# Kernel tuning notes

Hardware: AMD Instinct MI355X
Metric: run time of the kernel (lower is better)

The kernel has to match this reference:

```python
import jax, jax.numpy as jnp
import numpy as np
from jax import lax

N = 8192

def _conv(x, w, b):
    # x: NCHW, w: OIHW, valid conv stride 1
    y = lax.conv_general_dilated(x, w, (1, 1), 'VALID',
                                 dimension_numbers=('NCHW', 'OIHW', 'NCHW'))
    return y + b[None, :, None, None]

def _maxpool2(x):
    return lax.reduce_window(x, -jnp.inf, lax.max, (1, 1, 2, 2), (1, 1, 2, 2), 'VALID')

def setup_inputs() -> dict:
    key = jax.random.key(0)
    ks = jax.random.split(key, 13)
    def rn(k, shape, scale):
        return jax.random.normal(k, shape, dtype=jnp.float32) * scale
    inp = {}
    inp['x'] = jax.random.normal(ks[0], (N, 3, 32, 32), dtype=jnp.float32)
    inp['W1'] = rn(ks[1], (6, 3, 5, 5), 0.1)
    inp['b1'] = rn(ks[2], (6,), 0.1)
    inp['W2'] = rn(ks[3], (16, 6, 5, 5), 0.08)
    inp['b2'] = rn(ks[4], (16,), 0.1)
    inp['Wf1'] = rn(ks[5], (120, 400), 0.05)
    inp['bf1'] = rn(ks[6], (120,), 0.05)
    inp['Wf2'] = rn(ks[7], (84, 120), 0.09)
    inp['bf2'] = rn(ks[8], (84,), 0.09)
    inp['Wg'] = rn(ks[9], (10, 84), 0.1)    # GATConv fc weight (no bias)
    inp['attn_l'] = rn(ks[10], (10,), 0.3)  # a_l (src)
    inp['attn_r'] = rn(ks[11], (10,), 0.3)  # a_r (dst)
    inp['bg'] = rn(ks[12], (10,), 0.1)      # GATConv output bias
    return inp

def reference(x, W1, b1, W2, b2, Wf1, bf1, Wf2, bf2, Wg, attn_l, attn_r, bg):
    # CNN feature extractor (LeNet style)
    h = _maxpool2(jax.nn.relu(_conv(x, W1, b1)))   # [N,6,14,14]
    h = _maxpool2(jax.nn.relu(_conv(h, W2, b2)))   # [N,16,5,5]
    h = h.reshape(-1, 16 * 5 * 5)                  # [N,400]
    h = jax.nn.relu(h @ Wf1.T + bf1)               # [N,120]
    h = jax.nn.relu(h @ Wf2.T + bf2)               # [N,84]
    # Single-head GAT over fully-connected graph (incl. self-loops):
    # equivalent dense formulation of DGL GATConv(84,10,1)
    z = h @ Wg.T                                    # [N,10]
    el = z @ attn_l                                 # src scores [N]
    er = z @ attn_r                                 # dst scores [N]
    # e[i,j]: edge src=j -> dst=i
    e = jax.nn.leaky_relu(er[:, None] + el[None, :], negative_slope=0.2)  # [N,N]
    alpha = jax.nn.softmax(e, axis=1)               # softmax over incoming edges
    out = alpha @ z + bg                            # [N,10]
    return out
```

## Files before the change

### kernel.cpp

```cpp
#include <hip/hip_runtime.h>
#include <hip/hip_bf16.h>

typedef _Float16 half8 __attribute__((ext_vector_type(8)));
typedef __attribute__((aligned(8))) half8 half8_a8;
typedef float floatx4 __attribute__((ext_vector_type(4)));

#define LOG2E 1.44269504088896340736f

__device__ __forceinline__ float pool4_dpp(float v) {
  int s1 = __builtin_amdgcn_update_dpp(0, __float_as_int(v), 0xB1, 0xF, 0xF, true);
  float v1 = fmaxf(v, __int_as_float(s1));
  int s2 = __builtin_amdgcn_update_dpp(0, __float_as_int(v1), 0x4E, 0xF, 0xF, true);
  return fmaxf(v1, __int_as_float(s2));
}

__global__ __launch_bounds__(256) void k_prep(const float* __restrict__ Wf1,
    const float* __restrict__ Wf2, const float* __restrict__ Wg,
    const float* __restrict__ W1, const float* __restrict__ W2,
    _Float16* __restrict__ w1f, _Float16* __restrict__ w2f,
    _Float16* __restrict__ wgf, _Float16* __restrict__ B1,
    _Float16* __restrict__ B2M) {
  const int i = blockIdx.x * 256 + threadIdx.x;
  if (i < 53248) {
    const int n = i / 416, k = i - n * 416;
    w1f[i] = (_Float16)((n < 120 && k < 400) ? Wf1[n * 400 + k] : 0.f);
  } else if (i < 65536) {
    const int j = i - 53248;
    const int n = j >> 7, k = j & 127;
    w2f[j] = (_Float16)((n < 84 && k < 120) ? Wf2[n * 120 + k] : 0.f);
  } else if (i < 67072) {
    const int g = i - 65536;
    const int n = g / 96, k = g - n * 96;
    wgf[g] = (_Float16)((n < 10 && k < 84) ? Wg[n * 84 + k] : 0.f);
  } else if (i < 73216) {
    const int g = i - 67072;
    const int n = g / 192, k = g - n * 192;
    const int co = n >> 2, cy = (n >> 1) & 1, cx = n & 1;
    const int pidx = k >> 3, j = k & 7;
    const int r = pidx >> 2, ci = pidx & 3;
    float v = 0.f;
    if (co < 6 && ci < 3) {
      const int ky = r - cy, kx = j - cx;
      if (ky >= 0 && ky < 5 && kx >= 0 && kx < 5)
        v = W1[((co * 3 + ci) * 5 + ky) * 5 + kx];
    }
    B1[g] = (_Float16)v;
  } else if (i < 77312) {
    const int g = i - 73216;
    const int n = g >> 8, k = g & 255;
    float v = 0.f;
    if (k < 240) {
      const int ci = k / 40, rem = k - ci * 40, r = rem >> 3, j = rem & 7;
      if (j < 5) v = W2[((n * 6 + ci) * 5 + r) * 5 + j];
    }
    B2M[g] = (_Float16)v;
  }
}

__global__ __launch_bounds__(256) void k_convs(const float* __restrict__ x,
    const _Float16* __restrict__ B1, const float* __restrict__ b1,
    const _Float16* __restrict__ B2M, const float* __restrict__ b2,
    _Float16* __restrict__ h2) {
  __shared__ __align__(16) char sm[35808];
  _Float16* h1L = (_Float16*)(sm + 31104);
  const int t = threadIdx.x;
  const int n0 = blockIdx.x * 2;
  const int w4 = t >> 6, lane = t & 63;
  const int l16 = lane & 15, q = lane >> 4;

  const float4* x4 = (const float4*)(x + (size_t)n0 * 3072);
  for (int i = t; i < 1536; i += 256) {
    const float4 v = x4[i];
    const int img = (i >= 768);
    const int ii = i - img * 768;
    const int ci = ii >> 8, rem2 = ii & 255;
    const int y = rem2 >> 3, c = rem2 & 7;
    union { _Float16 h[2]; unsigned u; } p01, p23;
    p01.h[0] = (_Float16)v.x; p01.h[1] = (_Float16)v.y;
    p23.h[0] = (_Float16)v.z; p23.h[1] = (_Float16)v.w;
    char* row = sm + img * 15552 + ci * 5184 + y * 80;
    *(uint2*)(row + 8 * c) = make_uint2(p01.u, p23.u);
    *(unsigned*)(row + 2596 + 8 * c) = p01.u;
    *(unsigned*)(row + 2600 + 8 * c) = p23.u;
  }
  if (t < 192) {
    const int img = t / 96, tt = t - img * 96;
    const int ci = tt >> 5, y = tt & 31;
    *(unsigned*)(sm + img * 15552 + ci * 5184 + 2596 + y * 80 + 64) = 0u;
  }
  if (t < 32) {
    const int im = t >> 4;
    h2[(size_t)(n0 + im) * 416 + 400 + (t & 15)] = (_Float16)0.f;
  }
  __syncthreads();

  {
    const int img = w4 >> 1, wl = w4 & 1;
    const int px = l16;
    const int colOff = (px & 1) ? (2596 + 4 * px) : (4 * px);
    const char* base = sm + img * 15552 + ((q == 3) ? 0 : q * 5184) + colOff;
    half8 bfr[2][6];
#pragma unroll
    for (int nt = 0; nt < 2; nt++)
#pragma unroll
      for (int kc = 0; kc < 6; kc++)
        bfr[nt][kc] =
            *(const half8*)(B1 + (size_t)(nt * 16 + l16) * 192 + kc * 32 + q * 8);
    const int co_n = l16 >> 2;
    const int co1 = 4 + co_n;
    const float bias0 = b1[co_n];
    const float bias1 = (co1 < 6) ? b1[co1] : 0.f;
    const int py0 = wl * 7;
    const int py1 = py0 + 7;
    half8 a[6];
#pragma unroll
    for (int r = 0; r < 6; r++)
      a[r] = *(const half8_a8*)(base + (2 * py0 + r) * 80);
    _Float16* dstb = h1L + img * 1176;
    const bool store_lane = (l16 & 3) == 0;
    for (int py = py0; py < py1; ++py) {
      floatx4 acc0, acc1;
#pragma unroll
      for (int r = 0; r < 4; r++) { acc0[r] = 0.f; acc1[r] = 0.f; }
#pragma unroll
      for (int kc = 0; kc < 6; kc++) {
        acc0 = __builtin_amdgcn_mfma_f32_16x16x32_f16(a[kc], bfr[0][kc], acc0, 0, 0, 0);
        acc1 = __builtin_amdgcn_mfma_f32_16x16x32_f16(a[kc], bfr[1][kc], acc1, 0, 0, 0);
      }
      if (py < py1 - 1) {
        a[0] = a[2]; a[1] = a[3]; a[2] = a[4]; a[3] = a[5];
        a[4] = *(const half8_a8*)(base + (2 * py + 6) * 80);
        a[5] = *(const half8_a8*)(base + (2 * py + 7) * 80);
      }
      float p0[4], p1[4];
#pragma unroll
      for (int r = 0; r < 4; r++) {
        p0[r] = fmaxf(pool4_dpp(acc0[r]) + bias0, 0.f);
        p1[r] = fmaxf(pool4_dpp(acc1[r]) + bias1, 0.f);
      }
      if (store_lane) {
        union { _Float16 h[2]; unsigned u; } s01, s23;
        s01.h[0] = (_Float16)p0[0]; s01.h[1] = (_Float16)p0[1];
        s23.h[0] = (_Float16)p0[2]; s23.h[1] = (_Float16)p0[3];
        _Float16* dst = dstb + co_n * 196 + py * 14 + q * 4;
        *(unsigned*)dst = s01.u;
        if (q < 3) *(unsigned*)(dst + 2) = s23.u;
        if (co1 < 6) {
          union { _Float16 h[2]; unsigned u; } t01, t23;
          t01.h[0] = (_Float16)p1[0]; t01.h[1] = (_Float16)p1[1];
          t23.h[0] = (_Float16)p1[2]; t23.h[1] = (_Float16)p1[3];
          _Float16* dst1 = dstb + co1 * 196 + py * 14 + q * 4;
          *(unsigned*)dst1 = t01.u;
          if (q < 3) *(unsigned*)(dst1 + 2) = t23.u;
        }
      }
    }
  }
  __syncthreads();

  if (t < 168) {
    const int img = t / 84, rem = t - img * 84;
    const int ci = rem / 14, y = rem - ci * 14;
    const unsigned* src = (const unsigned*)(h1L + img * 1176 + ci * 196 + y * 14);
    unsigned u[10];
#pragma unroll
    for (int k = 0; k < 7; k++) u[k] = src[k];
    u[7] = 0u; u[8] = 0u; u[9] = 0u;
    char* base = sm + img * 11136 + ci * 1856 + y * 32;
#pragma unroll
    for (int ww = 0; ww < 8; ww++) {
      *(unsigned*)(base + 4 * ww) = u[ww];
      *(unsigned*)(base + 464 + 4 * ww) = (u[ww] >> 16) | (u[ww + 1] << 16);
      *(unsigned*)(base + 928 + 4 * ww) = u[ww + 1];
      *(unsigned*)(base + 1392 + 4 * ww) = (u[ww + 1] >> 16) | (u[ww + 2] << 16);
    }
  }
  __syncthreads();

  {
    int C2[8];
#pragma unroll
    for (int kc = 0; kc < 8; kc++) {
      const int pidx = kc * 4 + q;
      C2[kc] = (pidx < 30) ? (pidx / 5) * 1856 + (pidx % 5) * 32 : 0;
    }
    half8 bfr[8];
#pragma unroll
    for (int kc = 0; kc < 8; kc++)
      bfr[kc] = *(const half8*)(B2M + (size_t)l16 * 256 + kc * 32 + q * 8);
    const float bias = b2[l16];
    for (int mt = w4; mt < 13; mt += 4) {
      const int m = min(mt * 16 + l16, 199);
      const int pos = m >> 2, cy = (m >> 1) & 1, cx = m & 1;
      const int img = pos / 25, p = pos - img * 25;
      const int py = p / 5, px = p - py * 5;
      const int h = 2 * px + cx, s = h & 3;
      const char* base =
          sm + img * 11136 + s * 464 + (2 * py + cy) * 32 + (h - s) * 2;
      half8 a[8];
#pragma unroll
      for (int kc = 0; kc < 8; kc++) a[kc] = *(const half8_a8*)(base + C2[kc]);
      floatx4 acc;
#pragma unroll
      for (int r = 0; r < 4; r++) acc[r] = 0.f;
#pragma unroll
      for (int kc = 0; kc < 8; kc++)
        acc = __builtin_amdgcn_mfma_f32_16x16x32_f16(a[kc], bfr[kc], acc, 0, 0, 0);
      const float v = fmaxf(fmaxf(acc[0], acc[1]), fmaxf(acc[2], acc[3]));
      const int posL = mt * 4 + q;
      if (posL < 50) {
        const int im = posL / 25, pp = posL - im * 25;
        h2[(size_t)(n0 + im) * 416 + l16 * 25 + pp] =
            (_Float16)fmaxf(v + bias, 0.f);
      }
    }
  }
}

__global__ __launch_bounds__(256) void k_mlp(
    const _Float16* __restrict__ h2, const _Float16* __restrict__ w1,
    const float* __restrict__ bf1, const _Float16* __restrict__ w2,
    const float* __restrict__ bf2, const _Float16* __restrict__ wg,
    const float* __restrict__ al, const float* __restrict__ ar,
    _Float16* __restrict__ zT, float* __restrict__ el, float* __restrict__ er) {
  __shared__ __align__(16) _Float16 h3s[32 * 136];
  __shared__ __align__(16) _Float16 h4s[32 * 104];
  __shared__ float zs[32 * 17];
  const int t = threadIdx.x;
  const int w = t >> 6, lane = t & 63;
  const int l16 = lane & 15, q = lane >> 4;
  const int row0 = blockIdx.x * 32;
  for (int i = t; i < 2176; i += 256) ((float*)h3s)[i] = 0.f;
  for (int i = t; i < 1664; i += 256) ((float*)h4s)[i] = 0.f;
  const int rt = w & 1, cg = w >> 1;
  const int am = row0 + rt * 16 + l16;
  floatx4 acc[4];
#pragma unroll
  for (int ct = 0; ct < 4; ct++)
#pragma unroll
    for (int r = 0; r < 4; r++) acc[ct][r] = 0.f;
  const half8* Ag = (const half8*)(h2 + (size_t)am * 416 + q * 8);
  for (int kc = 0; kc < 13; kc++) {
    half8 a = Ag[kc * 4];
#pragma unroll
    for (int ct = 0; ct < 4; ct++) {
      const int n = cg * 64 + ct * 16 + l16;
      half8 b = *(const half8*)(w1 + (size_t)n * 416 + kc * 32 + q * 8);
      acc[ct] = __builtin_amdgcn_mfma_f32_16x16x32_f16(a, b, acc[ct], 0, 0, 0);
    }
  }
  __syncthreads();
#pragma unroll
  for (int ct = 0; ct < 4; ct++) {
    const int n = cg * 64 + ct * 16 + l16;
    if (n < 120) {
      const float bias = bf1[n];
#pragma unroll
      for (int r = 0; r < 4; r++) {
        const int rr = rt * 16 + q * 4 + r;
        h3s[rr * 136 + n] = (_Float16)fmaxf(acc[ct][r] + bias, 0.f);
      }
    }
  }
  __syncthreads();
  const int cbase2 = (w >> 1) * 3;
  floatx4 acc2[3];
#pragma unroll
  for (int ct = 0; ct < 3; ct++)
#pragma unroll
    for (int r = 0; r < 4; r++) acc2[ct][r] = 0.f;
  const _Float16* A2 = h3s + (rt * 16 + l16) * 136 + q * 8;
  for (int kc = 0; kc < 4; kc++) {
    half8 a = *(const half8*)(A2 + kc * 32);
#pragma unroll
    for (int ct = 0; ct < 3; ct++) {
      const int n = (cbase2 + ct) * 16 + l16;
      half8 b = *(const half8*)(w2 + (size_t)n * 128 + kc * 32 + q * 8);
      acc2[ct] = __builtin_amdgcn_mfma_f32_16x16x32_f16(a, b, acc2[ct], 0, 0, 0);
    }
  }
  __syncthreads();
#pragma unroll
  for (int ct = 0; ct < 3; ct++) {
    const int n = (cbase2 + ct) * 16 + l16;
    if (n < 84) {
      const float bias = bf2[n];
#pragma unroll
      for (int r = 0; r < 4; r++) {
        const int rr = rt * 16 + q * 4 + r;
        h4s[rr * 104 + n] = (_Float16)fmaxf(acc2[ct][r] + bias, 0.f);
      }
    }
  }
  __syncthreads();
  if (w < 2) {
    floatx4 acc3;
#pragma unroll
    for (int r = 0; r < 4; r++) acc3[r] = 0.f;
    const _Float16* A3 = h4s + (w * 16 + l16) * 104 + q * 8;
    for (int kc = 0; kc < 3; kc++) {
      half8 a = *(const half8*)(A3 + kc * 32);
      half8 b = *(const half8*)(wg + (size_t)l16 * 96 + kc * 32 + q * 8);
      acc3 = __builtin_amdgcn_mfma_f32_16x16x32_f16(a, b, acc3, 0, 0, 0);
    }
#pragma unroll
    for (int r = 0; r < 4; r++) {
      const int rr = w * 16 + q * 4 + r;
      zs[rr * 17 + l16] = acc3[r];
    }
  }
  __syncthreads();
  if (t < 32) {
    float e1 = 0.f, e2 = 0.f;
#pragma unroll
    for (int d = 0; d < 10; d++) {
      const float zv = zs[t * 17 + d];
      e1 += zv * al[d];
      e2 += zv * ar[d];
    }
    el[row0 + t] = e1 * LOG2E;
    er[row0 + t] = e2 * LOG2E;
  }
  for (int idx = t; idx < 352; idx += 256) {
    const int d = idx >> 5, c = idx & 31;
    zT[(size_t)d * 8192 + row0 + c] =
        (d < 10) ? (_Float16)zs[c * 17 + d] : (_Float16)1.0f;
  }
}

__global__ __launch_bounds__(256) void k_elmax(const float* __restrict__ el,
                                               float* __restrict__ out) {
  __shared__ float red[4];
  const int t = threadIdx.x;
  float m = -1e30f;
  for (int i = t; i < 8192; i += 256) m = fmaxf(m, el[i]);
#pragma unroll
  for (int off = 32; off > 0; off >>= 1) m = fmaxf(m, __shfl_down(m, off, 64));
  if ((t & 63) == 0) red[t >> 6] = m;
  __syncthreads();
  if (t == 0) out[0] = fmaxf(fmaxf(red[0], red[1]), fmaxf(red[2], red[3]));
}

__global__ __launch_bounds__(256) void k_attn(const _Float16* __restrict__ zT,
    const float* __restrict__ el, const float* __restrict__ er,
    const float* __restrict__ elmax, float* __restrict__ part) {
  const int t = threadIdx.x;
  const int w = t >> 6, lane = t & 63;
  const int l16 = lane & 15, q = lane >> 4;
  const int itile = blockIdx.x * 64 + w * 16;
  const int jb = blockIdx.y * 1024;
  const float mx = elmax[0];
  const float eri = er[itile + l16];
  const float s0 = eri + mx;
  const float mi = fmaxf(s0, 0.2f * s0);
  floatx4 acc;
#pragma unroll
  for (int r = 0; r < 4; r++) acc[r] = 0.f;
  const float* elp = el + jb + q * 8;
  const _Float16* ztp = zT + (size_t)l16 * 8192 + jb + q * 8;
  for (int jc = 0; jc < 32; jc++) {
    const float4 e0 = *(const float4*)(elp + jc * 32);
    const float4 e1 = *(const float4*)(elp + jc * 32 + 4);
    float wf[8];
    const float ej[8] = {e0.x, e0.y, e0.z, e0.w, e1.x, e1.y, e1.z, e1.w};
#pragma unroll
    for (int u = 0; u < 8; u++) {
      const float s = eri + ej[u];
      const float lr = fmaxf(s, 0.2f * s);
      wf[u] = exp2f(lr - mi);
    }
    half8 a;
#pragma unroll
    for (int u = 0; u < 8; u++) a[u] = (_Float16)wf[u];
    const half8 b = *(const half8*)(ztp + jc * 32);
    acc = __builtin_amdgcn_mfma_f32_16x16x32_f16(a, b, acc, 0, 0, 0);
  }
  if (l16 < 11) {
    float* pp = part + (size_t)blockIdx.y * 98304 + (size_t)l16 * 8192 + itile + q * 4;
#pragma unroll
    for (int r = 0; r < 4; r++) pp[r] = acc[r];
  }
}

__global__ __launch_bounds__(256) void k_final(const float* __restrict__ part,
    const float* __restrict__ bg, float* __restrict__ out) {
  __shared__ float red[8][32][12];
  const int t = threadIdx.x;
  const int i0 = blockIdx.x * 32;
  const int il = t & 31, sg = t >> 5;
  const float* pp = part + (size_t)sg * 98304 + i0 + il;
#pragma unroll
  for (int d = 0; d < 11; d++) red[sg][il][d] = pp[d * 8192];
  __syncthreads();
  for (int t2 = t; t2 < 352; t2 += 256) {
    const int ii = t2 / 11, d = t2 - ii * 11;
    if (d < 10) {
      float num = 0.f, den = 0.f;
#pragma unroll
      for (int s = 0; s < 8; s++) {
        num += red[s][ii][d];
        den += red[s][ii][10];
      }
      out[(size_t)(i0 + ii) * 10 + d] = num / den + bg[d];
    }
  }
}

extern "C" void kernel_launch(void* const* d_in, const int* in_sizes, int n_in,
                              void* d_out, int out_size, void* d_ws, size_t ws_size,
                              hipStream_t stream) {
  const float* x   = (const float*)d_in[0];
  const float* W1  = (const float*)d_in[1];
  const float* b1  = (const float*)d_in[2];
  const float* W2  = (const float*)d_in[3];
  const float* b2  = (const float*)d_in[4];
  const float* Wf1 = (const float*)d_in[5];
  const float* bf1 = (const float*)d_in[6];
  const float* Wf2 = (const float*)d_in[7];
  const float* bf2 = (const float*)d_in[8];
  const float* Wg  = (const float*)d_in[9];
  const float* al  = (const float*)d_in[10];
  const float* ar  = (const float*)d_in[11];
  const float* bg  = (const float*)d_in[12];
  float* out = (float*)d_out;

  float* ws = (float*)d_ws;
  float* p = ws + (size_t)8192 * 588;
  _Float16* h2f = (_Float16*)p;
  p += (size_t)8192 * 208;
  _Float16* zTf = (_Float16*)p; p += 65536;
  float* el  = p; p += 8192;
  float* er  = p; p += 8192;
  float* emx = p; p += 16;
  _Float16* w1f = (_Float16*)p; p += 26624;
  _Float16* w2f = (_Float16*)p; p += 6144;
  _Float16* wgf = (_Float16*)p; p += 768;
  _Float16* B1g = (_Float16*)p; p += 3072;
  _Float16* B2g = (_Float16*)p; p += 2048;
  float* part = ws;

  k_prep<<<302, 256, 0, stream>>>(Wf1, Wf2, Wg, W1, W2, w1f, w2f, wgf, B1g, B2g);
  k_convs<<<4096, 256, 0, stream>>>(x, B1g, b1, B2g, b2, h2f);
  k_mlp<<<256, 256, 0, stream>>>(h2f, w1f, bf1, w2f, bf2, wgf, al, ar, zTf, el, er);
  k_elmax<<<1, 256, 0, stream>>>(el, emx);
  dim3 ag(128, 8);
  k_attn<<<ag, 256, 0, stream>>>(zTf, el, er, emx, part);
  k_final<<<256, 256, 0, stream>>>(part, bg, out);
}
```

Baseline: 257.5 us.

## Fuse max, attention and final reduction; process four images per conv block

The separate el-max kernel is removed. The max is now computed inside the MLP kernel with a warp reduction and an atomicMax on a monotonic uint encoding, and the counter is reset in the prep kernel. The attention kernel now uses 1024-thread blocks that reduce the 8 j-slices in shared memory and write the final output directly, which drops the partials buffer and the final kernel. The conv kernel moves from 2 to 4 images per block with 512 threads and slightly padded shared-memory strides, which increases LDS use per block and may lower occupancy.

New measurement: 256.6 us. Within noise of the previous version (-0.3%).

```diff
diff --git a/kernel.cpp b/kernel.cpp
--- a/kernel.cpp
+++ b/kernel.cpp
@@ -14,13 +14,23 @@
   return fmaxf(v1, __int_as_float(s2));
 }
 
+__device__ __forceinline__ unsigned f2mono(float f) {
+  unsigned u = __float_as_uint(f);
+  return (u & 0x80000000u) ? ~u : (u | 0x80000000u);
+}
+__device__ __forceinline__ float mono2f(unsigned u) {
+  return (u & 0x80000000u) ? __uint_as_float(u & 0x7fffffffu)
+                           : __uint_as_float(~u);
+}
+
 __global__ __launch_bounds__(256) void k_prep(const float* __restrict__ Wf1,
     const float* __restrict__ Wf2, const float* __restrict__ Wg,
     const float* __restrict__ W1, const float* __restrict__ W2,
     _Float16* __restrict__ w1f, _Float16* __restrict__ w2f,
     _Float16* __restrict__ wgf, _Float16* __restrict__ B1,
-    _Float16* __restrict__ B2M) {
+    _Float16* __restrict__ B2M, unsigned* __restrict__ emx) {
   const int i = blockIdx.x * 256 + threadIdx.x;
+  if (i == 0) emx[0] = 0u;
   if (i < 53248) {
     const int n = i / 416, k = i - n * 416;
     w1f[i] = (_Float16)((n < 120 && k < 400) ? Wf1[n * 400 + k] : 0.f);
@@ -57,21 +67,21 @@
   }
 }
 
-__global__ __launch_bounds__(256) void k_convs(const float* __restrict__ x,
+__global__ __launch_bounds__(512) void k_convs(const float* __restrict__ x,
     const _Float16* __restrict__ B1, const float* __restrict__ b1,
     const _Float16* __restrict__ B2M, const float* __restrict__ b2,
     _Float16* __restrict__ h2) {
-  __shared__ __align__(16) char sm[35808];
-  _Float16* h1L = (_Float16*)(sm + 31104);
+  __shared__ __align__(16) char sm[71616];
+  _Float16* h1L = (_Float16*)(sm + 62208);
   const int t = threadIdx.x;
-  const int n0 = blockIdx.x * 2;
-  const int w4 = t >> 6, lane = t & 63;
+  const int n0 = blockIdx.x * 4;
+  const int w8 = t >> 6, lane = t & 63;
   const int l16 = lane & 15, q = lane >> 4;
 
   const float4* x4 = (const float4*)(x + (size_t)n0 * 3072);
-  for (int i = t; i < 1536; i += 256) {
+  for (int i = t; i < 3072; i += 512) {
     const float4 v = x4[i];
-    const int img = (i >= 768);
+    const int img = i / 768;
     const int ii = i - img * 768;
     const int ci = ii >> 8, rem2 = ii & 255;
     const int y = rem2 >> 3, c = rem2 & 7;
@@ -83,19 +93,19 @@
     *(unsigned*)(row + 2596 + 8 * c) = p01.u;
     *(unsigned*)(row + 2600 + 8 * c) = p23.u;
   }
-  if (t < 192) {
+  if (t < 384) {
     const int img = t / 96, tt = t - img * 96;
     const int ci = tt >> 5, y = tt & 31;
     *(unsigned*)(sm + img * 15552 + ci * 5184 + 2596 + y * 80 + 64) = 0u;
   }
-  if (t < 32) {
+  if (t < 64) {
     const int im = t >> 4;
     h2[(size_t)(n0 + im) * 416 + 400 + (t & 15)] = (_Float16)0.f;
   }
   __syncthreads();
 
   {
-    const int img = w4 >> 1, wl = w4 & 1;
+    const int img = w8 >> 1, wl = w8 & 1;
     const int px = l16;
     const int colOff = (px & 1) ? (2596 + 4 * px) : (4 * px);
     const char* base = sm + img * 15552 + ((q == 3) ? 0 : q * 5184) + colOff;
@@ -158,7 +168,7 @@
   }
   __syncthreads();
 
-  if (t < 168) {
+  if (t < 336) {
     const int img = t / 84, rem = t - img * 84;
     const int ci = rem / 14, y = rem - ci * 14;
     const unsigned* src = (const unsigned*)(h1L + img * 1176 + ci * 196 + y * 14);
@@ -166,7 +176,7 @@
 #pragma unroll
     for (int k = 0; k < 7; k++) u[k] = src[k];
     u[7] = 0u; u[8] = 0u; u[9] = 0u;
-    char* base = sm + img * 11136 + ci * 1856 + y * 32;
+    char* base = sm + img * 11184 + ci * 1864 + y * 32;
 #pragma unroll
     for (int ww = 0; ww < 8; ww++) {
       *(unsigned*)(base + 4 * ww) = u[ww];
@@ -182,21 +192,21 @@
 #pragma unroll
     for (int kc = 0; kc < 8; kc++) {
       const int pidx = kc * 4 + q;
-      C2[kc] = (pidx < 30) ? (pidx / 5) * 1856 + (pidx % 5) * 32 : 0;
+      C2[kc] = (pidx < 30) ? (pidx / 5) * 1864 + (pidx % 5) * 32 : 0;
     }
     half8 bfr[8];
 #pragma unroll
     for (int kc = 0; kc < 8; kc++)
       bfr[kc] = *(const half8*)(B2M + (size_t)l16 * 256 + kc * 32 + q * 8);
     const float bias = b2[l16];
-    for (int mt = w4; mt < 13; mt += 4) {
-      const int m = min(mt * 16 + l16, 199);
+    for (int mt = w8; mt < 26; mt += 8) {
+      const int m = min(mt * 16 + l16, 399);
       const int pos = m >> 2, cy = (m >> 1) & 1, cx = m & 1;
       const int img = pos / 25, p = pos - img * 25;
       const int py = p / 5, px = p - py * 5;
       const int h = 2 * px + cx, s = h & 3;
       const char* base =
-          sm + img * 11136 + s * 464 + (2 * py + cy) * 32 + (h - s) * 2;
+          sm + img * 11184 + s * 464 + (2 * py + cy) * 32 + (h - s) * 2;
       half8 a[8];
 #pragma unroll
       for (int kc = 0; kc < 8; kc++) a[kc] = *(const half8_a8*)(base + C2[kc]);
@@ -208,7 +218,7 @@
         acc = __builtin_amdgcn_mfma_f32_16x16x32_f16(a[kc], bfr[kc], acc, 0, 0, 0);
       const float v = fmaxf(fmaxf(acc[0], acc[1]), fmaxf(acc[2], acc[3]));
       const int posL = mt * 4 + q;
-      if (posL < 50) {
+      if (posL < 100) {
         const int im = posL / 25, pp = posL - im * 25;
         h2[(size_t)(n0 + im) * 416 + l16 * 25 + pp] =
             (_Float16)fmaxf(v + bias, 0.f);
@@ -222,7 +232,8 @@
     const float* __restrict__ bf1, const _Float16* __restrict__ w2,
     const float* __restrict__ bf2, const _Float16* __restrict__ wg,
     const float* __restrict__ al, const float* __restrict__ ar,
-    _Float16* __restrict__ zT, float* __restrict__ el, float* __restrict__ er) {
+    _Float16* __restrict__ zT, float* __restrict__ el, float* __restrict__ er,
+    unsigned* __restrict__ emx) {
   __shared__ __align__(16) _Float16 h3s[32 * 136];
   __shared__ __align__(16) _Float16 h4s[32 * 104];
   __shared__ float zs[32 * 17];
@@ -318,8 +329,14 @@
       e1 += zv * al[d];
       e2 += zv * ar[d];
     }
-    el[row0 + t] = e1 * LOG2E;
+    const float elv = e1 * LOG2E;
+    el[row0 + t] = elv;
     er[row0 + t] = e2 * LOG2E;
+    float m = elv;
+#pragma unroll
+    for (int off = 16; off > 0; off >>= 1)
+      m = fmaxf(m, __shfl_down(m, off, 32));
+    if (t == 0) atomicMax(emx, f2mono(m));
   }
   for (int idx = t; idx < 352; idx += 256) {
     const int d = idx >> 5, c = idx & 31;
@@ -328,28 +345,19 @@
   }
 }
 
-__global__ __launch_bounds__(256) void k_elmax(const float* __restrict__ el,
-                                               float* __restrict__ out) {
-  __shared__ float red[4];
-  const int t = threadIdx.x;
-  float m = -1e30f;
-  for (int i = t; i < 8192; i += 256) m = fmaxf(m, el[i]);
-#pragma unroll
-  for (int off = 32; off > 0; off >>= 1) m = fmaxf(m, __shfl_down(m, off, 64));
-  if ((t & 63) == 0) red[t >> 6] = m;
-  __syncthreads();
-  if (t == 0) out[0] = fmaxf(fmaxf(red[0], red[1]), fmaxf(red[2], red[3]));
-}
-
-__global__ __launch_bounds__(256) void k_attn(const _Float16* __restrict__ zT,
+__global__ __launch_bounds__(1024) void k_attn(const _Float16* __restrict__ zT,
     const float* __restrict__ el, const float* __restrict__ er,
-    const float* __restrict__ elmax, float* __restrict__ part) {
+    const unsigned* __restrict__ emx, const float* __restrict__ bg,
+    float* __restrict__ out) {
+  __shared__ float red[8][2][16][12];
   const int t = threadIdx.x;
   const int w = t >> 6, lane = t & 63;
   const int l16 = lane & 15, q = lane >> 4;
-  const int itile = blockIdx.x * 64 + w * 16;
-  const int jb = blockIdx.y * 1024;
-  const float mx = elmax[0];
+  const int isub = w & 1, js = w >> 1;
+  const int row0 = blockIdx.x * 32;
+  const int itile = row0 + isub * 16;
+  const int jb = js * 1024;
+  const float mx = mono2f(emx[0]);
   const float eri = er[itile + l16];
   const float s0 = eri + mx;
   const float mi = fmaxf(s0, 0.2f * s0);
@@ -376,33 +384,20 @@
     acc = __builtin_amdgcn_mfma_f32_16x16x32_f16(a, b, acc, 0, 0, 0);
   }
   if (l16 < 11) {
-    float* pp = part + (size_t)blockIdx.y * 98304 + (size_t)l16 * 8192 + itile + q * 4;
-#pragma unroll
-    for (int r = 0; r < 4; r++) pp[r] = acc[r];
-  }
-}
-
-__global__ __launch_bounds__(256) void k_final(const float* __restrict__ part,
-    const float* __restrict__ bg, float* __restrict__ out) {
-  __shared__ float red[8][32][12];
-  const int t = threadIdx.x;
-  const int i0 = blockIdx.x * 32;
-  const int il = t & 31, sg = t >> 5;
-  const float* pp = part + (size_t)sg * 98304 + i0 + il;
-#pragma unroll
-  for (int d = 0; d < 11; d++) red[sg][il][d] = pp[d * 8192];
-  __syncthreads();
-  for (int t2 = t; t2 < 352; t2 += 256) {
-    const int ii = t2 / 11, d = t2 - ii * 11;
-    if (d < 10) {
-      float num = 0.f, den = 0.f;
-#pragma unroll
-      for (int s = 0; s < 8; s++) {
-        num += red[s][ii][d];
-        den += red[s][ii][10];
-      }
-      out[(size_t)(i0 + ii) * 10 + d] = num / den + bg[d];
-    }
+#pragma unroll
+    for (int r = 0; r < 4; r++) red[js][isub][q * 4 + r][l16] = acc[r];
+  }
+  __syncthreads();
+  if (t < 320) {
+    const int ii = t / 10, d = t - (t / 10) * 10;
+    const int i1 = ii >> 4, i2 = ii & 15;
+    float num = 0.f, den = 0.f;
+#pragma unroll
+    for (int s = 0; s < 8; s++) {
+      num += red[s][i1][i2][d];
+      den += red[s][i1][i2][10];
+    }
+    out[(size_t)(row0 + ii) * 10 + d] = num / den + bg[d];
   }
 }
 
@@ -431,19 +426,15 @@
   _Float16* zTf = (_Float16*)p; p += 65536;
   float* el  = p; p += 8192;
   float* er  = p; p += 8192;
-  float* emx = p; p += 16;
+  unsigned* emx = (unsigned*)p; p += 16;
   _Float16* w1f = (_Float16*)p; p += 26624;
   _Float16* w2f = (_Float16*)p; p += 6144;
   _Float16* wgf = (_Float16*)p; p += 768;
   _Float16* B1g = (_Float16*)p; p += 3072;
   _Float16* B2g = (_Float16*)p; p += 2048;
-  float* part = ws;
-
-  k_prep<<<302, 256, 0, stream>>>(Wf1, Wf2, Wg, W1, W2, w1f, w2f, wgf, B1g, B2g);
-  k_convs<<<4096, 256, 0, stream>>>(x, B1g, b1, B2g, b2, h2f);
-  k_mlp<<<256, 256, 0, stream>>>(h2f, w1f, bf1, w2f, bf2, wgf, al, ar, zTf, el, er);
-  k_elmax<<<1, 256, 0, stream>>>(el, emx);
-  dim3 ag(128, 8);
-  k_attn<<<ag, 256, 0, stream>>>(zTf, el, er, emx, part);
-  k_final<<<256, 256, 0, stream>>>(part, bg, out);
-}
+
+  k_prep<<<302, 256, 0, stream>>>(Wf1, Wf2, Wg, W1, W2, w1f, w2f, wgf, B1g, B2g, emx);
+  k_convs<<<2048, 512, 0, stream>>>(x, B1g, b1, B2g, b2, h2f);
+  k_mlp<<<256, 256, 0, stream>>>(h2f, w1f, bf1, w2f, bf2, wgf, al, ar, zTf, el, er, emx);
+  k_attn<<<256, 1024, 0, stream>>>(zTf, el, er, emx, bg, out);
+}
```
